# Performance work log

Measured on AMD Instinct MI355X. Metric: run time of the kernel, lower is better.

The kernel has to match this reference:

```python
import jax, jax.numpy as jnp
import numpy as np

B, T, DIM = 2, 2048, 2048
N_HEAD, N_GROUP = 16, 4
KV_HEAD = N_HEAD // N_GROUP
HEAD_DIM = DIM // N_HEAD


def setup_inputs() -> dict:
    key = jax.random.key(0)
    ks = jax.random.split(key, 7)
    x = jax.random.normal(ks[0], (B, T, DIM), dtype=jnp.float32)
    # rotary tables: last dim = head_dim // 2 (interleaved real/imag pairs)
    pos = jnp.arange(T, dtype=jnp.float32)[:, None]
    inv_freq = 1.0 / (10000.0 ** (jnp.arange(0, HEAD_DIM, 2, dtype=jnp.float32) / HEAD_DIM))
    angles = pos * inv_freq[None, :]  # [T, HEAD_DIM//2]
    freqs_cos = jnp.cos(angles)
    freqs_sin = jnp.sin(angles)
    scale = 0.02
    wq = jax.random.normal(ks[1], (DIM, N_HEAD * HEAD_DIM), dtype=jnp.float32) * scale
    wk = jax.random.normal(ks[2], (DIM, KV_HEAD * HEAD_DIM), dtype=jnp.float32) * scale
    wv = jax.random.normal(ks[3], (DIM, KV_HEAD * HEAD_DIM), dtype=jnp.float32) * scale
    wo = jax.random.normal(ks[4], (N_HEAD * HEAD_DIM, DIM), dtype=jnp.float32) * scale
    return {"x": x, "freqs_cos": freqs_cos, "freqs_sin": freqs_sin,
            "wq": wq, "wk": wk, "wv": wv, "wo": wo}


def _apply_rope(t, cos, sin):
    # t: [B, T, H, D]; interleaved pairs (..., -1, 2) as in torch reference
    tr = t.reshape(*t.shape[:-1], -1, 2)
    r, i = tr[..., 0], tr[..., 1]
    c = cos[None, :, None, :]  # [1, T, 1, D//2]
    s = sin[None, :, None, :]
    out = jnp.stack([r * c - i * s, r * s + i * c], axis=-1)
    return out.reshape(t.shape)


def reference(x, freqs_cos, freqs_sin, wq, wk, wv, wo):
    Bx, Tx, C = x.shape
    xq = (x @ wq).reshape(Bx, Tx, N_HEAD, HEAD_DIM)
    xk = (x @ wk).reshape(Bx, Tx, KV_HEAD, HEAD_DIM)
    xv = (x @ wv).reshape(Bx, Tx, KV_HEAD, HEAD_DIM)
    xq = _apply_rope(xq, freqs_cos, freqs_sin)
    xk = _apply_rope(xk, freqs_cos, freqs_sin)
    # repeat_kv: each kv head repeated n_group times consecutively
    xk = jnp.repeat(xk, N_GROUP, axis=2)  # [B, T, N_HEAD, D]
    xv = jnp.repeat(xv, N_GROUP, axis=2)
    scale = HEAD_DIM ** -0.5
    att = jnp.einsum('bqhd,bkhd->bhqk', xq, xk) * scale
    causal = jnp.tril(jnp.ones((Tx, Tx), dtype=bool))
    att = jnp.where(causal[None, None], att, -jnp.inf)
    att = jax.nn.softmax(att, axis=-1)
    out = jnp.einsum('bhqk,bkhd->bqhd', att, xv).reshape(Bx, Tx, N_HEAD * HEAD_DIM)
    return out @ wo
```

## Files before the change

### kernel.cpp

```cpp
#include <hip/hip_runtime.h>

#define TB 2
#define TT 2048
#define TDIM 2048
#define NHEADS 16
#define KVHEADS 4
#define HD 128

typedef unsigned short u16;
typedef unsigned int u32;
typedef __attribute__((ext_vector_type(8))) short short8;
typedef __attribute__((ext_vector_type(4))) float float4_t;

__device__ __forceinline__ float b2f(u16 u) {
    union { u32 i; float f; } v; v.i = ((u32)u) << 16; return v.f;
}
__device__ __forceinline__ u16 f2b(float f) {
    union { float f; u32 i; } v; v.f = f;
    u32 r = (v.i + 0x7FFFu + ((v.i >> 16) & 1u)) >> 16;
    return (u16)r;
}
__device__ __forceinline__ u32 fbits(float f) {
    union { float f; u32 i; } v; v.f = f; return v.i;
}

__device__ __forceinline__ void gl_lds16(const void* g, void* l) {
    __builtin_amdgcn_global_load_lds((const __attribute__((address_space(1))) void*)g,
                                     (__attribute__((address_space(3))) void*)l, 16, 0, 0);
}

template <bool F32OUT, bool ROPE>
__global__ __launch_bounds__(256, 3)
void gemm_bt(const u16* __restrict__ A, const u16* __restrict__ BT,
             void* __restrict__ Cv, int M, int N, int K,
             const float* __restrict__ fc, const float* __restrict__ fs) {
    __shared__ __align__(16) u16 As[128 * 64];
    __shared__ __align__(16) u16 Bs[128 * 64];
    const int tid  = threadIdx.x;
    const int wave = tid >> 6, lane = tid & 63;
    const int quad = lane >> 4, l16 = lane & 15;
    const int wm = wave >> 1, wn = wave & 1;
    const int row0 = blockIdx.y * 128, col0 = blockIdx.x * 128;

    float4_t acc[4][4];
#pragma unroll
    for (int i = 0; i < 4; i++)
#pragma unroll
        for (int j = 0; j < 4; j++) acc[i][j] = (float4_t){0.f, 0.f, 0.f, 0.f};

    for (int kk = 0; kk < K; kk += 64) {
        __syncthreads();
#pragma unroll
        for (int i = 0; i < 4; i++) {
            int n = i * 256 + wave * 64 + lane;
            int r = n >> 3, c = (n & 7) ^ (r & 7);
            gl_lds16(A  + (size_t)(row0 + r) * K + kk + c * 8, &As[(i * 256 + wave * 64) * 8]);
            gl_lds16(BT + (size_t)(col0 + r) * K + kk + c * 8, &Bs[(i * 256 + wave * 64) * 8]);
        }
        __syncthreads();
#pragma unroll
        for (int ks = 0; ks < 2; ks++) {
            short8 af[4], bf[4];
#pragma unroll
            for (int mt = 0; mt < 4; mt++) {
                int m = wm * 64 + mt * 16 + l16;
                af[mt] = *(const short8*)&As[(m * 8 + ((ks * 4 + quad) ^ (l16 & 7))) * 8];
            }
#pragma unroll
            for (int nt = 0; nt < 4; nt++) {
                int n = wn * 64 + nt * 16 + l16;
                bf[nt] = *(const short8*)&Bs[(n * 8 + ((ks * 4 + quad) ^ (l16 & 7))) * 8];
            }
#pragma unroll
            for (int mt = 0; mt < 4; mt++)
#pragma unroll
                for (int nt = 0; nt < 4; nt++)
                    acc[mt][nt] = __builtin_amdgcn_mfma_f32_16x16x32_bf16(
                        af[mt], bf[nt], acc[mt][nt], 0, 0, 0);
        }
    }
    const bool do_rope = ROPE && (col0 < 2560);
#pragma unroll
    for (int mt = 0; mt < 4; mt++)
#pragma unroll
        for (int nt = 0; nt < 4; nt++)
#pragma unroll
            for (int r = 0; r < 4; r++) {
                int row = row0 + wm * 64 + mt * 16 + quad * 4 + r;
                int col = col0 + wn * 64 + nt * 16 + l16;
                float v = acc[mt][nt][r];
                if (ROPE && do_rope) {
                    float other = __shfl_xor(v, 1, 64);
                    int t = row & (TT - 1);
                    int i0 = (col & (HD - 1)) >> 1;
                    float c = fc[t * 64 + i0], s = fs[t * 64 + i0];
                    v = (col & 1) ? fmaf(v, c, other * s) : fmaf(v, c, -other * s);
                }
                if (F32OUT)
                    ((float*)Cv)[(size_t)row * N + col] = v;
                else
                    ((u16*)Cv)[(size_t)row * N + col] = f2b(v);
            }
}

__global__ void cvt_transpose(const float* __restrict__ in, u16* __restrict__ out,
                              int rows, int cols) {
    __shared__ u16 tile[32][33];
    int c0 = blockIdx.x * 32, r0 = blockIdx.y * 32;
    int tx = threadIdx.x & 31, ty = threadIdx.x >> 5;
#pragma unroll
    for (int i = 0; i < 4; i++)
        tile[ty + i * 8][tx] = f2b(in[(size_t)(r0 + ty + i * 8) * cols + c0 + tx]);
    __syncthreads();
#pragma unroll
    for (int i = 0; i < 4; i++)
        out[(size_t)(c0 + ty + i * 8) * rows + r0 + tx] = tile[tx][ty + i * 8];
}

__global__ void cvt_bf16(const float* __restrict__ in, u16* __restrict__ out) {
    size_t i = ((size_t)blockIdx.x * 256 + threadIdx.x) * 4;
    float4 v = *(const float4*)(in + i);
    ushort4 o;
    o.x = f2b(v.x); o.y = f2b(v.y); o.z = f2b(v.z); o.w = f2b(v.w);
    *(ushort4*)(out + i) = o;
}

__global__ void transpose_v(const u16* __restrict__ QKV, u16* __restrict__ Vt) {
    int z = blockIdx.z, b = z >> 2, kv = z & 3;
    const u16* in = QKV + (size_t)b * TT * 3072 + 2560 + kv * HD;
    u16* out = Vt + (size_t)z * HD * TT;
    __shared__ u16 tile[32][33];
    int t0 = blockIdx.x * 32, d0 = blockIdx.y * 32;
    int tx = threadIdx.x & 31, ty = threadIdx.x >> 5;
#pragma unroll
    for (int i = 0; i < 4; i++)
        tile[ty + i * 8][tx] = in[(size_t)(t0 + ty + i * 8) * 3072 + d0 + tx];
    __syncthreads();
#pragma unroll
    for (int i = 0; i < 4; i++)
        out[(size_t)(d0 + ty + i * 8) * TT + t0 + tx] = tile[tx][ty + i * 8];
}

#define PSTR 72
__global__ __launch_bounds__(256, 1)
void attn(const u16* __restrict__ QKV, const u16* __restrict__ Vt,
          u16* __restrict__ O) {
    const int g  = blockIdx.x;
    const int yp = blockIdx.y;
    const int b  = blockIdx.z;
    const int kvh = yp >> 1;
    const int hb  = kvh * 4 + (yp & 1) * 2;
    const int tid = threadIdx.x, w = tid >> 6, lane = tid & 63;
    const int quad = lane >> 4, l16 = lane & 15;

    __shared__ __align__(16) u16 Ks[2][64 * 128];
    __shared__ __align__(16) u16 Vs[2][128 * 64];
    __shared__ __align__(16) u16 Ps[8][16 * PSTR];

    const u16* Kbase = QKV + (size_t)b * TT * 3072 + 2048 + kvh * HD;
    const u16* Vbase = Vt + (size_t)(b * 4 + kvh) * HD * TT;
    const float Cl = 0.12753102474f;

    auto stage = [&](int kt, int bb) {
#pragma unroll
        for (int i = 0; i < 4; i++) {
            int n = i * 256 + w * 64 + lane;
            int r = n >> 4, c = (n & 15) ^ (r & 15);
            gl_lds16(Kbase + (size_t)(kt * 64 + r) * 3072 + c * 8,
                     &Ks[bb][(i * 256 + w * 64) * 8]);
        }
#pragma unroll
        for (int i = 0; i < 4; i++) {
            int n = i * 256 + w * 64 + lane;
            int d = n >> 3, c = (n & 7) ^ (d & 7);
            gl_lds16(Vbase + (size_t)d * TT + kt * 64 + c * 8,
                     &Vs[bb][(i * 256 + w * 64) * 8]);
        }
    };

    for (int ph = 0; ph < 2; ph++) {
        const int qb = ph ? (31 - g) : g;
        __syncthreads();
        stage(0, 0);

        short8 qf[2][4];
#pragma unroll
        for (int hd = 0; hd < 2; hd++) {
            const u16* Qrow = QKV + ((size_t)b * TT + qb * 64 + w * 16 + l16) * 3072
                              + (hb + hd) * HD;
#pragma unroll
            for (int ks = 0; ks < 4; ks++)
                qf[hd][ks] = *(const short8*)(Qrow + ks * 32 + quad * 8);
        }

        float4_t o[2][8];
#pragma unroll
        for (int hd = 0; hd < 2; hd++)
#pragma unroll
            for (int i = 0; i < 8; i++) o[hd][i] = (float4_t){0.f, 0.f, 0.f, 0.f};
        float mi[2] = {-1e30f, -1e30f}, li[2] = {0.f, 0.f};
        const int qg = qb * 64 + w * 16 + l16;

        for (int kt = 0; kt <= qb; kt++) {
            const int cur = kt & 1;
            __syncthreads();
            if (kt < qb) stage(kt + 1, cur ^ 1);

            float4_t st[2][4];
#pragma unroll
            for (int hd = 0; hd < 2; hd++)
#pragma unroll
                for (int nt = 0; nt < 4; nt++) st[hd][nt] = (float4_t){0.f, 0.f, 0.f, 0.f};
#pragma unroll
            for (int ks = 0; ks < 4; ks++) {
                short8 af[4];
#pragma unroll
                for (int nt = 0; nt < 4; nt++)
                    af[nt] = *(const short8*)&Ks[cur][((nt * 16 + l16) * 16 +
                                                      ((ks * 4 + quad) ^ l16)) * 8];
#pragma unroll
                for (int nt = 0; nt < 4; nt++) {
                    st[0][nt] = __builtin_amdgcn_mfma_f32_16x16x32_bf16(
                        af[nt], qf[0][ks], st[0][nt], 0, 0, 0);
                    st[1][nt] = __builtin_amdgcn_mfma_f32_16x16x32_bf16(
                        af[nt], qf[1][ks], st[1][nt], 0, 0, 0);
                }
            }

            const bool diag = (kt == qb);
            float alpha[2];
#pragma unroll
            for (int hd = 0; hd < 2; hd++) {
                if (diag) {
#pragma unroll
                    for (int nt = 0; nt < 4; nt++)
#pragma unroll
                        for (int r = 0; r < 4; r++) {
                            int key = kt * 64 + nt * 16 + quad * 4 + r;
                            if (key > qg) st[hd][nt][r] = -3e38f;
                        }
                }
                float pm = -3e38f;
#pragma unroll
                for (int nt = 0; nt < 4; nt++)
#pragma unroll
                    for (int r = 0; r < 4; r++) pm = fmaxf(pm, st[hd][nt][r]);
                pm = fmaxf(pm, __shfl_xor(pm, 16, 64));
                pm = fmaxf(pm, __shfl_xor(pm, 32, 64));
                float mnew = fmaxf(mi[hd], pm);
                alpha[hd] = __builtin_amdgcn_exp2f((mi[hd] - mnew) * Cl);
                mi[hd] = mnew;
                const float mC = mnew * Cl;
                float rs = 0.f;
#pragma unroll
                for (int nt = 0; nt < 4; nt++)
#pragma unroll
                    for (int r = 0; r < 4; r++) {
                        float e = __builtin_amdgcn_exp2f(fmaf(st[hd][nt][r], Cl, -mC));
                        st[hd][nt][r] = e;
                        rs += e;
                    }
                rs += __shfl_xor(rs, 16, 64);
                rs += __shfl_xor(rs, 32, 64);
                li[hd] = li[hd] * alpha[hd] + rs;

#pragma unroll
                for (int nt = 0; nt < 4; nt++) {
                    uint2 pk;
                    pk.x = __builtin_amdgcn_perm(fbits(st[hd][nt][1]), fbits(st[hd][nt][0]), 0x07060302u);
                    pk.y = __builtin_amdgcn_perm(fbits(st[hd][nt][3]), fbits(st[hd][nt][2]), 0x07060302u);
                    *(uint2*)&Ps[w * 2 + hd][l16 * PSTR + nt * 16 + quad * 4] = pk;
                }
                float a_o[4];
#pragma unroll
                for (int r = 0; r < 4; r++) a_o[r] = __shfl(alpha[hd], quad * 4 + r, 64);
#pragma unroll
                for (int n2 = 0; n2 < 8; n2++)
#pragma unroll
                    for (int r = 0; r < 4; r++) o[hd][n2][r] *= a_o[r];
            }

#pragma unroll
            for (int ks2 = 0; ks2 < 2; ks2++) {
                short8 apA = *(const short8*)&Ps[w * 2 + 0][l16 * PSTR + ks2 * 32 + quad * 8];
                short8 apB = *(const short8*)&Ps[w * 2 + 1][l16 * PSTR + ks2 * 32 + quad * 8];
#pragma unroll
                for (int n2 = 0; n2 < 8; n2++) {
                    short8 bv = *(const short8*)&Vs[cur][((n2 * 16 + l16) * 8 +
                                                         ((ks2 * 4 + quad) ^ (l16 & 7))) * 8];
                    o[0][n2] = __builtin_amdgcn_mfma_f32_16x16x32_bf16(apA, bv, o[0][n2], 0, 0, 0);
                    o[1][n2] = __builtin_amdgcn_mfma_f32_16x16x32_bf16(apB, bv, o[1][n2], 0, 0, 0);
                }
            }
        }

#pragma unroll
        for (int hd = 0; hd < 2; hd++) {
            float l_o[4];
#pragma unroll
            for (int r = 0; r < 4; r++) l_o[r] = __shfl(li[hd], quad * 4 + r, 64);
            u16* Ob2 = O + ((size_t)b * TT + qb * 64 + w * 16) * TDIM + (hb + hd) * HD;
#pragma unroll
            for (int n2 = 0; n2 < 8; n2++)
#pragma unroll
                for (int r = 0; r < 4; r++)
                    Ob2[(size_t)(quad * 4 + r) * TDIM + n2 * 16 + l16] =
                        f2b(o[hd][n2][r] / l_o[r]);
        }
    }
}

extern "C" void kernel_launch(void* const* d_in, const int* in_sizes, int n_in,
                              void* d_out, int out_size, void* d_ws, size_t ws_size,
                              hipStream_t stream) {
    const float* x  = (const float*)d_in[0];
    const float* fc = (const float*)d_in[1];
    const float* fs = (const float*)d_in[2];
    const float* wq = (const float*)d_in[3];
    const float* wk = (const float*)d_in[4];
    const float* wv = (const float*)d_in[5];
    const float* wo = (const float*)d_in[6];
    float* out = (float*)d_out;

    char* ws = (char*)d_ws;
    size_t off = 0;
    auto alloc = [&](size_t bytes) -> void* {
        void* p = ws + off;
        off += (bytes + 255) & ~(size_t)255;
        return p;
    };
    u16* xb  = (u16*)alloc((size_t)4096 * 2048 * 2);
    u16* WT  = (u16*)alloc((size_t)3072 * 2048 * 2);
    u16* woT = (u16*)alloc((size_t)2048 * 2048 * 2);
    u16* QKV = (u16*)alloc((size_t)4096 * 3072 * 2);
    u16* Vtb = (u16*)alloc((size_t)4096 * 512 * 2);
    u16* Ob  = (u16*)alloc((size_t)4096 * 2048 * 2);

    dim3 blk(256);
    cvt_bf16<<<dim3(8192), blk, 0, stream>>>(x, xb);
    cvt_transpose<<<dim3(64, 64), blk, 0, stream>>>(wq, WT, 2048, 2048);
    cvt_transpose<<<dim3(16, 64), blk, 0, stream>>>(wk, WT + (size_t)2048 * 2048, 2048, 512);
    cvt_transpose<<<dim3(16, 64), blk, 0, stream>>>(wv, WT + (size_t)2560 * 2048, 2048, 512);
    cvt_transpose<<<dim3(64, 64), blk, 0, stream>>>(wo, woT, 2048, 2048);
    gemm_bt<false, true><<<dim3(24, 32), blk, 0, stream>>>(
        xb, WT, QKV, 4096, 3072, 2048, fc, fs);
    transpose_v<<<dim3(64, 4, 8), blk, 0, stream>>>(QKV, Vtb);
    attn<<<dim3(16, 8, 2), blk, 0, stream>>>(QKV, Vtb, Ob);
    gemm_bt<true, false><<<dim3(16, 32), blk, 0, stream>>>(
        Ob, woT, out, 4096, 2048, 2048, nullptr, nullptr);
}
```

Before: 321.6 us.

## Split attention blocks per q-tile, single-buffer V, fuse weight transposes

```diff
diff --git a/kernel.cpp b/kernel.cpp
--- a/kernel.cpp
+++ b/kernel.cpp
@@ -103,10 +103,18 @@
             }
 }
 
-__global__ void cvt_transpose(const float* __restrict__ in, u16* __restrict__ out,
-                              int rows, int cols) {
+__global__ void cvt_transpose4(const float* __restrict__ wq, const float* __restrict__ wk,
+                               const float* __restrict__ wv, const float* __restrict__ wo,
+                               u16* __restrict__ WT, u16* __restrict__ woT) {
+    int bx = blockIdx.x;
+    const float* in; u16* out; int cols, cx;
+    if (bx < 64)      { in = wq; out = WT;                         cols = 2048; cx = bx; }
+    else if (bx < 80) { in = wk; out = WT + (size_t)2048 * 2048;   cols = 512;  cx = bx - 64; }
+    else if (bx < 96) { in = wv; out = WT + (size_t)2560 * 2048;   cols = 512;  cx = bx - 80; }
+    else              { in = wo; out = woT;                        cols = 2048; cx = bx - 96; }
+    const int rows = 2048;
     __shared__ u16 tile[32][33];
-    int c0 = blockIdx.x * 32, r0 = blockIdx.y * 32;
+    int c0 = cx * 32, r0 = blockIdx.y * 32;
     int tx = threadIdx.x & 31, ty = threadIdx.x >> 5;
 #pragma unroll
     for (int i = 0; i < 4; i++)
@@ -142,26 +150,28 @@
 }
 
 #define PSTR 72
-__global__ __launch_bounds__(256, 1)
+__global__ __launch_bounds__(256, 2)
 void attn(const u16* __restrict__ QKV, const u16* __restrict__ Vt,
           u16* __restrict__ O) {
-    const int g  = blockIdx.x;
-    const int yp = blockIdx.y;
-    const int b  = blockIdx.z;
-    const int kvh = yp >> 1;
-    const int hb  = kvh * 4 + (yp & 1) * 2;
+    const int x  = blockIdx.x;
+    const int y  = blockIdx.y;
+    const int b  = y >> 3;
+    const int hp = y & 7;
+    const int kvh = hp >> 1;
+    const int hb  = kvh * 4 + (hp & 1) * 2;
+    const int qb  = b ? (31 - x) : x;
     const int tid = threadIdx.x, w = tid >> 6, lane = tid & 63;
     const int quad = lane >> 4, l16 = lane & 15;
 
     __shared__ __align__(16) u16 Ks[2][64 * 128];
-    __shared__ __align__(16) u16 Vs[2][128 * 64];
+    __shared__ __align__(16) u16 Vs[128 * 64];
     __shared__ __align__(16) u16 Ps[8][16 * PSTR];
 
     const u16* Kbase = QKV + (size_t)b * TT * 3072 + 2048 + kvh * HD;
     const u16* Vbase = Vt + (size_t)(b * 4 + kvh) * HD * TT;
     const float Cl = 0.12753102474f;
 
-    auto stage = [&](int kt, int bb) {
+    auto stageK = [&](int kt, int bb) {
 #pragma unroll
         for (int i = 0; i < 4; i++) {
             int n = i * 256 + w * 64 + lane;
@@ -169,144 +179,145 @@
             gl_lds16(Kbase + (size_t)(kt * 64 + r) * 3072 + c * 8,
                      &Ks[bb][(i * 256 + w * 64) * 8]);
         }
+    };
+    auto stageV = [&](int kt) {
 #pragma unroll
         for (int i = 0; i < 4; i++) {
             int n = i * 256 + w * 64 + lane;
             int d = n >> 3, c = (n & 7) ^ (d & 7);
             gl_lds16(Vbase + (size_t)d * TT + kt * 64 + c * 8,
-                     &Vs[bb][(i * 256 + w * 64) * 8]);
+                     &Vs[(i * 256 + w * 64) * 8]);
         }
     };
 
-    for (int ph = 0; ph < 2; ph++) {
-        const int qb = ph ? (31 - g) : g;
+    stageK(0, 0);
+
+    short8 qf[2][4];
+#pragma unroll
+    for (int hd = 0; hd < 2; hd++) {
+        const u16* Qrow = QKV + ((size_t)b * TT + qb * 64 + w * 16 + l16) * 3072
+                          + (hb + hd) * HD;
+#pragma unroll
+        for (int ks = 0; ks < 4; ks++)
+            qf[hd][ks] = *(const short8*)(Qrow + ks * 32 + quad * 8);
+    }
+
+    float4_t o[2][8];
+#pragma unroll
+    for (int hd = 0; hd < 2; hd++)
+#pragma unroll
+        for (int i = 0; i < 8; i++) o[hd][i] = (float4_t){0.f, 0.f, 0.f, 0.f};
+    float mi[2] = {-1e30f, -1e30f}, li[2] = {0.f, 0.f};
+    const int qg = qb * 64 + w * 16 + l16;
+
+    for (int kt = 0; kt <= qb; kt++) {
+        const int cur = kt & 1;
         __syncthreads();
-        stage(0, 0);
-
-        short8 qf[2][4];
+        stageV(kt);
+
+        float4_t st[2][4];
+#pragma unroll
+        for (int hd = 0; hd < 2; hd++)
+#pragma unroll
+            for (int nt = 0; nt < 4; nt++) st[hd][nt] = (float4_t){0.f, 0.f, 0.f, 0.f};
+#pragma unroll
+        for (int ks = 0; ks < 4; ks++) {
+            short8 af[4];
+#pragma unroll
+            for (int nt = 0; nt < 4; nt++)
+                af[nt] = *(const short8*)&Ks[cur][((nt * 16 + l16) * 16 +
+                                                  ((ks * 4 + quad) ^ l16)) * 8];
+#pragma unroll
+            for (int nt = 0; nt < 4; nt++) {
+                st[0][nt] = __builtin_amdgcn_mfma_f32_16x16x32_bf16(
+                    af[nt], qf[0][ks], st[0][nt], 0, 0, 0);
+                st[1][nt] = __builtin_amdgcn_mfma_f32_16x16x32_bf16(
+                    af[nt], qf[1][ks], st[1][nt], 0, 0, 0);
+            }
+        }
+
+        const bool diag = (kt == qb);
+        float alpha[2];
 #pragma unroll
         for (int hd = 0; hd < 2; hd++) {
-            const u16* Qrow = QKV + ((size_t)b * TT + qb * 64 + w * 16 + l16) * 3072
-                              + (hb + hd) * HD;
-#pragma unroll
-            for (int ks = 0; ks < 4; ks++)
-                qf[hd][ks] = *(const short8*)(Qrow + ks * 32 + quad * 8);
-        }
-
-        float4_t o[2][8];
-#pragma unroll
-        for (int hd = 0; hd < 2; hd++)
-#pragma unroll
-            for (int i = 0; i < 8; i++) o[hd][i] = (float4_t){0.f, 0.f, 0.f, 0.f};
-        float mi[2] = {-1e30f, -1e30f}, li[2] = {0.f, 0.f};
-        const int qg = qb * 64 + w * 16 + l16;
-
-        for (int kt = 0; kt <= qb; kt++) {
-            const int cur = kt & 1;
-            __syncthreads();
-            if (kt < qb) stage(kt + 1, cur ^ 1);
-
-            float4_t st[2][4];
-#pragma unroll
-            for (int hd = 0; hd < 2; hd++)
-#pragma unroll
-                for (int nt = 0; nt < 4; nt++) st[hd][nt] = (float4_t){0.f, 0.f, 0.f, 0.f};
-#pragma unroll
-            for (int ks = 0; ks < 4; ks++) {
-                short8 af[4];
+            if (diag) {
 #pragma unroll
                 for (int nt = 0; nt < 4; nt++)
-                    af[nt] = *(const short8*)&Ks[cur][((nt * 16 + l16) * 16 +
-                                                      ((ks * 4 + quad) ^ l16)) * 8];
-#pragma unroll
-                for (int nt = 0; nt < 4; nt++) {
-                    st[0][nt] = __builtin_amdgcn_mfma_f32_16x16x32_bf16(
-                        af[nt], qf[0][ks], st[0][nt], 0, 0, 0);
-                    st[1][nt] = __builtin_amdgcn_mfma_f32_16x16x32_bf16(
-                        af[nt], qf[1][ks], st[1][nt], 0, 0, 0);
+#pragma unroll
+                    for (int r = 0; r < 4; r++) {
+                        int key = kt * 64 + nt * 16 + quad * 4 + r;
+                        if (key > qg) st[hd][nt][r] = -3e38f;
+                    }
+            }
+            float pm = -3e38f;
+#pragma unroll
+            for (int nt = 0; nt < 4; nt++)
+#pragma unroll
+                for (int r = 0; r < 4; r++) pm = fmaxf(pm, st[hd][nt][r]);
+            pm = fmaxf(pm, __shfl_xor(pm, 16, 64));
+            pm = fmaxf(pm, __shfl_xor(pm, 32, 64));
+            float mnew = fmaxf(mi[hd], pm);
+            alpha[hd] = __builtin_amdgcn_exp2f((mi[hd] - mnew) * Cl);
+            mi[hd] = mnew;
+            const float mC = mnew * Cl;
+            float rs = 0.f;
+#pragma unroll
+            for (int nt = 0; nt < 4; nt++)
+#pragma unroll
+                for (int r = 0; r < 4; r++) {
+                    float e = __builtin_amdgcn_exp2f(fmaf(st[hd][nt][r], Cl, -mC));
+                    st[hd][nt][r] = e;
+                    rs += e;
                 }
-            }
-
-            const bool diag = (kt == qb);
-            float alpha[2];
-#pragma unroll
-            for (int hd = 0; hd < 2; hd++) {
-                if (diag) {
-#pragma unroll
-                    for (int nt = 0; nt < 4; nt++)
-#pragma unroll
-                        for (int r = 0; r < 4; r++) {
-                            int key = kt * 64 + nt * 16 + quad * 4 + r;
-                            if (key > qg) st[hd][nt][r] = -3e38f;
-                        }
-                }
-                float pm = -3e38f;
-#pragma unroll
-                for (int nt = 0; nt < 4; nt++)
-#pragma unroll
-                    for (int r = 0; r < 4; r++) pm = fmaxf(pm, st[hd][nt][r]);
-                pm = fmaxf(pm, __shfl_xor(pm, 16, 64));
-                pm = fmaxf(pm, __shfl_xor(pm, 32, 64));
-                float mnew = fmaxf(mi[hd], pm);
-                alpha[hd] = __builtin_amdgcn_exp2f((mi[hd] - mnew) * Cl);
-                mi[hd] = mnew;
-                const float mC = mnew * Cl;
-                float rs = 0.f;
-#pragma unroll
-                for (int nt = 0; nt < 4; nt++)
-#pragma unroll
-                    for (int r = 0; r < 4; r++) {
-                        float e = __builtin_amdgcn_exp2f(fmaf(st[hd][nt][r], Cl, -mC));
-                        st[hd][nt][r] = e;
-                        rs += e;
-                    }
-                rs += __shfl_xor(rs, 16, 64);
-                rs += __shfl_xor(rs, 32, 64);
-                li[hd] = li[hd] * alpha[hd] + rs;
-
-#pragma unroll
-                for (int nt = 0; nt < 4; nt++) {
-                    uint2 pk;
-                    pk.x = __builtin_amdgcn_perm(fbits(st[hd][nt][1]), fbits(st[hd][nt][0]), 0x07060302u);
-                    pk.y = __builtin_amdgcn_perm(fbits(st[hd][nt][3]), fbits(st[hd][nt][2]), 0x07060302u);
-                    *(uint2*)&Ps[w * 2 + hd][l16 * PSTR + nt * 16 + quad * 4] = pk;
-                }
-                float a_o[4];
-#pragma unroll
-                for (int r = 0; r < 4; r++) a_o[r] = __shfl(alpha[hd], quad * 4 + r, 64);
-#pragma unroll
-                for (int n2 = 0; n2 < 8; n2++)
-#pragma unroll
-                    for (int r = 0; r < 4; r++) o[hd][n2][r] *= a_o[r];
-            }
-
-#pragma unroll
-            for (int ks2 = 0; ks2 < 2; ks2++) {
-                short8 apA = *(const short8*)&Ps[w * 2 + 0][l16 * PSTR + ks2 * 32 + quad * 8];
-                short8 apB = *(const short8*)&Ps[w * 2 + 1][l16 * PSTR + ks2 * 32 + quad * 8];
-#pragma unroll
-                for (int n2 = 0; n2 < 8; n2++) {
-                    short8 bv = *(const short8*)&Vs[cur][((n2 * 16 + l16) * 8 +
-                                                         ((ks2 * 4 + quad) ^ (l16 & 7))) * 8];
-                    o[0][n2] = __builtin_amdgcn_mfma_f32_16x16x32_bf16(apA, bv, o[0][n2], 0, 0, 0);
-                    o[1][n2] = __builtin_amdgcn_mfma_f32_16x16x32_bf16(apB, bv, o[1][n2], 0, 0, 0);
-                }
-            }
-        }
-
-#pragma unroll
-        for (int hd = 0; hd < 2; hd++) {
-            float l_o[4];
-#pragma unroll
-            for (int r = 0; r < 4; r++) l_o[r] = __shfl(li[hd], quad * 4 + r, 64);
-            u16* Ob2 = O + ((size_t)b * TT + qb * 64 + w * 16) * TDIM + (hb + hd) * HD;
+            rs += __shfl_xor(rs, 16, 64);
+            rs += __shfl_xor(rs, 32, 64);
+            li[hd] = li[hd] * alpha[hd] + rs;
+
+#pragma unroll
+            for (int nt = 0; nt < 4; nt++) {
+                uint2 pk;
+                pk.x = __builtin_amdgcn_perm(fbits(st[hd][nt][1]), fbits(st[hd][nt][0]), 0x07060302u);
+                pk.y = __builtin_amdgcn_perm(fbits(st[hd][nt][3]), fbits(st[hd][nt][2]), 0x07060302u);
+                *(uint2*)&Ps[w * 2 + hd][l16 * PSTR + nt * 16 + quad * 4] = pk;
+            }
+            float a_o[4];
+#pragma unroll
+            for (int r = 0; r < 4; r++) a_o[r] = __shfl(alpha[hd], quad * 4 + r, 64);
 #pragma unroll
             for (int n2 = 0; n2 < 8; n2++)
 #pragma unroll
-                for (int r = 0; r < 4; r++)
-                    Ob2[(size_t)(quad * 4 + r) * TDIM + n2 * 16 + l16] =
-                        f2b(o[hd][n2][r] / l_o[r]);
-        }
+                for (int r = 0; r < 4; r++) o[hd][n2][r] *= a_o[r];
+        }
+
+        __syncthreads();
+        if (kt < qb) stageK(kt + 1, cur ^ 1);
+
+#pragma unroll
+        for (int ks2 = 0; ks2 < 2; ks2++) {
+            short8 apA = *(const short8*)&Ps[w * 2 + 0][l16 * PSTR + ks2 * 32 + quad * 8];
+            short8 apB = *(const short8*)&Ps[w * 2 + 1][l16 * PSTR + ks2 * 32 + quad * 8];
+#pragma unroll
+            for (int n2 = 0; n2 < 8; n2++) {
+                short8 bv = *(const short8*)&Vs[((n2 * 16 + l16) * 8 +
+                                                ((ks2 * 4 + quad) ^ (l16 & 7))) * 8];
+                o[0][n2] = __builtin_amdgcn_mfma_f32_16x16x32_bf16(apA, bv, o[0][n2], 0, 0, 0);
+                o[1][n2] = __builtin_amdgcn_mfma_f32_16x16x32_bf16(apB, bv, o[1][n2], 0, 0, 0);
+            }
+        }
+    }
+
+#pragma unroll
+    for (int hd = 0; hd < 2; hd++) {
+        float l_o[4];
+#pragma unroll
+        for (int r = 0; r < 4; r++) l_o[r] = __shfl(li[hd], quad * 4 + r, 64);
+        u16* Ob2 = O + ((size_t)b * TT + qb * 64 + w * 16) * TDIM + (hb + hd) * HD;
+#pragma unroll
+        for (int n2 = 0; n2 < 8; n2++)
+#pragma unroll
+            for (int r = 0; r < 4; r++)
+                Ob2[(size_t)(quad * 4 + r) * TDIM + n2 * 16 + l16] =
+                    f2b(o[hd][n2][r] / l_o[r]);
     }
 }
 
@@ -338,14 +349,11 @@
 
     dim3 blk(256);
     cvt_bf16<<<dim3(8192), blk, 0, stream>>>(x, xb);
-    cvt_transpose<<<dim3(64, 64), blk, 0, stream>>>(wq, WT, 2048, 2048);
-    cvt_transpose<<<dim3(16, 64), blk, 0, stream>>>(wk, WT + (size_t)2048 * 2048, 2048, 512);
-    cvt_transpose<<<dim3(16, 64), blk, 0, stream>>>(wv, WT + (size_t)2560 * 2048, 2048, 512);
-    cvt_transpose<<<dim3(64, 64), blk, 0, stream>>>(wo, woT, 2048, 2048);
+    cvt_transpose4<<<dim3(160, 64), blk, 0, stream>>>(wq, wk, wv, wo, WT, woT);
     gemm_bt<false, true><<<dim3(24, 32), blk, 0, stream>>>(
         xb, WT, QKV, 4096, 3072, 2048, fc, fs);
     transpose_v<<<dim3(64, 4, 8), blk, 0, stream>>>(QKV, Vtb);
-    attn<<<dim3(16, 8, 2), blk, 0, stream>>>(QKV, Vtb, Ob);
+    attn<<<dim3(32, 16), blk, 0, stream>>>(QKV, Vtb, Ob);
     gemm_bt<true, false><<<dim3(16, 32), blk, 0, stream>>>(
         Ob, woT, out, 4096, 2048, 2048, nullptr, nullptr);
 }
```

Result: faster. 291.4 us (-9.4%).
